# Performance work log

Measured on AMD Instinct MI355X. Metric: run time of the kernel, lower is better.

## Reference

```python
import jax, jax.numpy as jnp
import numpy as np
import math

D_MODEL = 512
N_HEADS = 8
WINDOW = 5
B, S = 4, 2048


def setup_inputs() -> dict:
    key = jax.random.key(0)
    ks = jax.random.split(key, 16)
    d = D_MODEL

    def lin(k, fan_in, fan_out):
        bound = 1.0 / math.sqrt(fan_in)
        kw, kb = jax.random.split(k)
        W = jax.random.uniform(kw, (fan_in, fan_out), jnp.float32, -bound, bound)
        b = jax.random.uniform(kb, (fan_out,), jnp.float32, -bound, bound)
        return W, b

    x = jax.random.normal(ks[0], (B, S, d), jnp.float32)
    W1, b1 = lin(ks[1], d, 2 * d)      # mapping layer 1
    W2, b2 = lin(ks[2], 2 * d, d)      # mapping layer 2
    Wq, bq = lin(ks[3], d, d)
    Wk, bk = lin(ks[4], d, d)
    Wv, bv = lin(ks[5], d, d)
    Wo, bo = lin(ks[6], d, d)
    return dict(x=x, W1=W1, b1=b1, W2=W2, b2=b2, Wq=Wq, bq=bq,
                Wk=Wk, bk=bk, Wv=Wv, bv=bv, Wo=Wo, bo=bo)


def reference(x, W1, b1, W2, b2, Wq, bq, Wk, bk, Wv, bv, Wo, bo):
    Bsz, S_, d = x.shape
    h = N_HEADS
    hd = d // h

    # mapping MLP: Linear -> ReLU -> Linear
    xm = jax.nn.relu(x @ W1 + b1) @ W2 + b2

    def split_heads(t):  # [B,S,d] -> [B,h,S,hd]
        return t.reshape(Bsz, S_, h, hd).transpose(0, 2, 1, 3)

    Q = split_heads(xm @ Wq + bq)
    K = split_heads(xm @ Wk + bk)
    V = split_heads(xm @ Wv + bv)

    scores = jnp.einsum('bhqd,bhkd->bhqk', Q, K) / math.sqrt(hd)

    # inverse sliding-window mask: positions with |i-j| <= window are EXCLUDED
    idx = jnp.arange(S_)
    adjacent = jnp.abs(idx[:, None] - idx[None, :]) <= WINDOW  # [S,S] bool
    scores = jnp.where(adjacent[None, None], -1e9, scores)

    attn = jax.nn.softmax(scores, axis=-1)
    out = jnp.einsum('bhqk,bhkd->bhqd', attn, V)
    out = out.transpose(0, 2, 1, 3).reshape(Bsz, S_, d)
    return out @ Wo + bo
```

## Files before the change

### kernel.cpp

```cpp
#include <hip/hip_runtime.h>
#include <stdint.h>

typedef __attribute__((ext_vector_type(8))) short bf16x8;
typedef __attribute__((ext_vector_type(4))) float f32x4;

__device__ __forceinline__ float bf2f(uint16_t u) {
    union { uint32_t u; float f; } c; c.u = ((uint32_t)u) << 16; return c.f;
}
__device__ __forceinline__ uint16_t f2bf(float f) {
    union { float f; uint32_t u; } c; c.f = f;
    uint32_t r = c.u + 0x7fffu + ((c.u >> 16) & 1u);
    return (uint16_t)(r >> 16);
}
__device__ __forceinline__ uint32_t pk2bf(float a, float b) {
#if __has_builtin(__builtin_amdgcn_cvt_pk_bf16_f32)
    auto v = __builtin_amdgcn_cvt_pk_bf16_f32(a, b);
    uint32_t u; __builtin_memcpy(&u, &v, 4); return u;
#else
    return (uint32_t)f2bf(a) | ((uint32_t)f2bf(b) << 16);
#endif
}
__device__ __forceinline__ float fexp2(float x) {
#if __has_builtin(__builtin_amdgcn_exp2f)
    return __builtin_amdgcn_exp2f(x);
#else
    return exp2f(x);
#endif
}

__device__ __forceinline__ void gld_lds16(const uint16_t* g, uint16_t* l) {
    __builtin_amdgcn_global_load_lds(
        (const __attribute__((address_space(1))) void*)g,
        (__attribute__((address_space(3))) void*)l, 16, 0, 0);
}

__global__ void prep_all(const float* __restrict__ x,
                         const float* __restrict__ W1, const float* __restrict__ W2,
                         const float* __restrict__ Wq, const float* __restrict__ Wk,
                         const float* __restrict__ Wv, const float* __restrict__ Wo,
                         const float* __restrict__ b1, const float* __restrict__ b2,
                         const float* __restrict__ bq, const float* __restrict__ bk,
                         const float* __restrict__ bv, const float* __restrict__ bo,
                         uint16_t* __restrict__ W1T, uint16_t* __restrict__ W2T,
                         uint16_t* __restrict__ WqkvT, uint16_t* __restrict__ WoT,
                         uint16_t* __restrict__ xb, uint16_t* __restrict__ bbase)
{
    const int id = blockIdx.x;
    const int tx = threadIdx.x, ty = threadIdx.y;
    const int tid = ty * 32 + tx;
    if (id < 2048) {
        __shared__ uint16_t t[32][33];
        const float* src; uint16_t* dst; int R, C, tile;
        if      (id < 512)  { src = W1; dst = W1T;              R = 512;  C = 1024; tile = id; }
        else if (id < 1024) { src = W2; dst = W2T;              R = 1024; C = 512;  tile = id - 512; }
        else if (id < 1280) { src = Wq; dst = WqkvT;            R = 512;  C = 512;  tile = id - 1024; }
        else if (id < 1536) { src = Wk; dst = WqkvT + 512*512;  R = 512;  C = 512;  tile = id - 1280; }
        else if (id < 1792) { src = Wv; dst = WqkvT + 1024*512; R = 512;  C = 512;  tile = id - 1536; }
        else                { src = Wo; dst = WoT;              R = 512;  C = 512;  tile = id - 1792; }
        const int ntx = C / 32;
        const int bx = (tile % ntx) * 32, by = (tile / ntx) * 32;
#pragma unroll
        for (int i = ty; i < 32; i += 8) t[i][tx] = f2bf(src[(size_t)(by + i) * C + bx + tx]);
        __syncthreads();
#pragma unroll
        for (int i = ty; i < 32; i += 8) dst[(size_t)(bx + i) * R + by + tx] = t[tx][i];
    } else if (id < 6144) {
        int i = (id - 2048) * 256 + tid;
        float4 v = ((const float4*)x)[i];
        ushort4 o;
        o.x = f2bf(v.x); o.y = f2bf(v.y); o.z = f2bf(v.z); o.w = f2bf(v.w);
        ((ushort4*)xb)[i] = o;
    } else {
        int i = (id - 6144) * 256 + tid;
        if      (i < 1024) bbase[i] = f2bf(b1[i]);
        else if (i < 1536) bbase[i] = f2bf(b2[i - 1024]);
        else if (i < 2048) bbase[i] = f2bf(bq[i - 1536]);
        else if (i < 2560) bbase[i] = f2bf(bk[i - 2048]);
        else if (i < 3072) bbase[i] = f2bf(bv[i - 2560]);
        else if (i < 3584) bbase[i] = f2bf(bo[i - 3072]);
    }
}

template<int RELU, int F32OUT>
__global__ __launch_bounds__(256)
void gemm_k(const uint16_t* __restrict__ A, const uint16_t* __restrict__ Bt,
            const uint16_t* __restrict__ bias, void* __restrict__ Cv,
            int M, int N, int K)
{
    __shared__ __align__(16) uint16_t lsA[128 * 64];
    __shared__ __align__(16) uint16_t lsB[128 * 64];

    const int tid = threadIdx.x, lane = tid & 63;
    const int wid = tid >> 6;
    const int quad = lane >> 4, lm = lane & 15;
    const int wm = wid >> 1, wn = wid & 1;
    const int m0 = blockIdx.y * 128, n0 = blockIdx.x * 128;

    f32x4 acc[4][4];
#pragma unroll
    for (int i = 0; i < 4; ++i)
#pragma unroll
        for (int j = 0; j < 4; ++j) acc[i][j] = (f32x4){0.f, 0.f, 0.f, 0.f};

    for (int k0 = 0; k0 < K; k0 += 64) {
        __syncthreads();
#pragma unroll
        for (int c4 = 0; c4 < 4; ++c4) {
            const int chunk = c4 * 256 + tid;
            const int r = chunk >> 3, lc = (chunk & 7) ^ (r & 7);
            gld_lds16(A  + (size_t)(m0 + r) * K + k0 + lc * 8, lsA + (size_t)chunk * 8);
            gld_lds16(Bt + (size_t)(n0 + r) * K + k0 + lc * 8, lsB + (size_t)chunk * 8);
        }
        __syncthreads();

#pragma unroll
        for (int kh = 0; kh < 2; ++kh) {
            bf16x8 af[4], bfr[4];
#pragma unroll
            for (int t = 0; t < 4; ++t) {
                const int pcA = ((kh * 4 + quad) ^ (lm & 7));
                af[t]  = *(const bf16x8*)(lsA + (wm * 64 + t * 16 + lm) * 64 + pcA * 8);
                bfr[t] = *(const bf16x8*)(lsB + (wn * 64 + t * 16 + lm) * 64 + pcA * 8);
            }
#pragma unroll
            for (int i = 0; i < 4; ++i)
#pragma unroll
                for (int j = 0; j < 4; ++j)
                    acc[i][j] = __builtin_amdgcn_mfma_f32_16x16x32_bf16(af[i], bfr[j], acc[i][j], 0, 0, 0);
        }
    }

#pragma unroll
    for (int i = 0; i < 4; ++i) {
        const int r0 = m0 + wm * 64 + i * 16 + quad * 4;
#pragma unroll
        for (int j = 0; j < 4; ++j) {
            const int col = n0 + wn * 64 + j * 16 + lm;
            const float bvj = bf2f(bias[col]);
#pragma unroll
            for (int r = 0; r < 4; ++r) {
                float v = acc[i][j][r] + bvj;
                if (RELU) v = fmaxf(v, 0.f);
                if (F32OUT) ((float*)Cv)[(size_t)(r0 + r) * N + col] = v;
                else        ((uint16_t*)Cv)[(size_t)(r0 + r) * N + col] = f2bf(v);
            }
        }
    }
}

template<int RELU, int F32OUT>
__global__ __launch_bounds__(256)
void gemm_k64(const uint16_t* __restrict__ A, const uint16_t* __restrict__ Bt,
              const uint16_t* __restrict__ bias, void* __restrict__ Cv,
              int M, int N, int K)
{
    __shared__ __align__(16) uint16_t lsA[64 * 64];
    __shared__ __align__(16) uint16_t lsB[128 * 64];

    const int tid = threadIdx.x, lane = tid & 63;
    const int wid = tid >> 6;
    const int quad = lane >> 4, lm = lane & 15;
    const int wm = wid >> 1, wn = wid & 1;
    const int m0 = blockIdx.y * 64, n0 = blockIdx.x * 128;

    f32x4 acc[2][4];
#pragma unroll
    for (int i = 0; i < 2; ++i)
#pragma unroll
        for (int j = 0; j < 4; ++j) acc[i][j] = (f32x4){0.f, 0.f, 0.f, 0.f};

    for (int k0 = 0; k0 < K; k0 += 64) {
        __syncthreads();
#pragma unroll
        for (int c4 = 0; c4 < 2; ++c4) {
            const int chunk = c4 * 256 + tid;
            const int r = chunk >> 3, lc = (chunk & 7) ^ (r & 7);
            gld_lds16(A + (size_t)(m0 + r) * K + k0 + lc * 8, lsA + (size_t)chunk * 8);
        }
#pragma unroll
        for (int c4 = 0; c4 < 4; ++c4) {
            const int chunk = c4 * 256 + tid;
            const int r = chunk >> 3, lc = (chunk & 7) ^ (r & 7);
            gld_lds16(Bt + (size_t)(n0 + r) * K + k0 + lc * 8, lsB + (size_t)chunk * 8);
        }
        __syncthreads();

#pragma unroll
        for (int kh = 0; kh < 2; ++kh) {
            const int pc = ((kh * 4 + quad) ^ (lm & 7));
            bf16x8 af[2], bfr[4];
#pragma unroll
            for (int t = 0; t < 2; ++t)
                af[t] = *(const bf16x8*)(lsA + (wm * 32 + t * 16 + lm) * 64 + pc * 8);
#pragma unroll
            for (int t = 0; t < 4; ++t)
                bfr[t] = *(const bf16x8*)(lsB + (wn * 64 + t * 16 + lm) * 64 + pc * 8);
#pragma unroll
            for (int i = 0; i < 2; ++i)
#pragma unroll
                for (int j = 0; j < 4; ++j)
                    acc[i][j] = __builtin_amdgcn_mfma_f32_16x16x32_bf16(af[i], bfr[j], acc[i][j], 0, 0, 0);
        }
    }

#pragma unroll
    for (int i = 0; i < 2; ++i) {
        const int r0 = m0 + wm * 32 + i * 16 + quad * 4;
#pragma unroll
        for (int j = 0; j < 4; ++j) {
            const int col = n0 + wn * 64 + j * 16 + lm;
            const float bvj = bf2f(bias[col]);
#pragma unroll
            for (int r = 0; r < 4; ++r) {
                float v = acc[i][j][r] + bvj;
                if (RELU) v = fmaxf(v, 0.f);
                if (F32OUT) ((float*)Cv)[(size_t)(r0 + r) * N + col] = v;
                else        ((uint16_t*)Cv)[(size_t)(r0 + r) * N + col] = f2bf(v);
            }
        }
    }
}

__global__ __launch_bounds__(256)
void gemm_qkv_s(const uint16_t* __restrict__ A, const uint16_t* __restrict__ Bt,
                const uint16_t* __restrict__ bq, const uint16_t* __restrict__ bk,
                const uint16_t* __restrict__ bv_,
                uint16_t* __restrict__ qk, uint16_t* __restrict__ Vt)
{
    __shared__ __align__(16) uint16_t lsA[128 * 64];
    __shared__ __align__(16) uint16_t lsB[128 * 64];

    const int tid = threadIdx.x, lane = tid & 63;
    const int wid = tid >> 6;
    const int quad = lane >> 4, lm = lane & 15;
    const int wm = wid >> 1, wn = wid & 1;
    const int m0 = blockIdx.y * 128, n0 = blockIdx.x * 128;
    const int part = n0 >> 9;
    const uint16_t* B = (part == 0) ? bq : (part == 1) ? bk : bv_;
    const int K = 512;

    f32x4 acc[4][4];
#pragma unroll
    for (int i = 0; i < 4; ++i)
#pragma unroll
        for (int j = 0; j < 4; ++j) acc[i][j] = (f32x4){0.f, 0.f, 0.f, 0.f};

    for (int k0 = 0; k0 < K; k0 += 64) {
        __syncthreads();
#pragma unroll
        for (int c4 = 0; c4 < 4; ++c4) {
            const int chunk = c4 * 256 + tid;
            const int r = chunk >> 3, lc = (chunk & 7) ^ (r & 7);
            gld_lds16(A  + (size_t)(m0 + r) * K + k0 + lc * 8, lsA + (size_t)chunk * 8);
            gld_lds16(Bt + (size_t)(n0 + r) * K + k0 + lc * 8, lsB + (size_t)chunk * 8);
        }
        __syncthreads();

#pragma unroll
        for (int kh = 0; kh < 2; ++kh) {
            const int pc = ((kh * 4 + quad) ^ (lm & 7));
            bf16x8 af[4], bfr[4];
#pragma unroll
            for (int t = 0; t < 4; ++t) {
                af[t]  = *(const bf16x8*)(lsA + (wm * 64 + t * 16 + lm) * 64 + pc * 8);
                bfr[t] = *(const bf16x8*)(lsB + (wn * 64 + t * 16 + lm) * 64 + pc * 8);
            }
#pragma unroll
            for (int i = 0; i < 4; ++i)
#pragma unroll
                for (int j = 0; j < 4; ++j)
                    acc[i][j] = __builtin_amdgcn_mfma_f32_16x16x32_bf16(af[i], bfr[j], acc[i][j], 0, 0, 0);
        }
    }

#pragma unroll
    for (int i = 0; i < 4; ++i) {
        const int mb = m0 + wm * 64 + i * 16 + quad * 4;
#pragma unroll
        for (int j = 0; j < 4; ++j) {
            const int nl = (n0 & 511) + wn * 64 + j * 16 + lm;
            const float bvj = bf2f(B[nl]);
            if (part < 2) {
#pragma unroll
                for (int r = 0; r < 4; ++r)
                    qk[(size_t)(mb + r) * 1024 + part * 512 + nl] = f2bf(acc[i][j][r] + bvj);
            } else {
                const int h = nl >> 6, d = nl & 63;
                const int b = mb >> 11, s0 = mb & 2047;
                const int sp = (s0 & ~31) | ((s0 & 12) << 1) | (((s0 >> 4) & 1) << 2);
                const size_t base = ((size_t)(((b << 3) | h)) * 64 + d) * 2048 + sp;
#pragma unroll
                for (int r = 0; r < 4; ++r)
                    Vt[base + r] = f2bf(acc[i][j][r] + bvj);
            }
        }
    }
}

__global__ __launch_bounds__(256, 3)
void attn_k(const uint16_t* __restrict__ qk, const uint16_t* __restrict__ Vt,
            uint16_t* __restrict__ Out)
{
    __shared__ __align__(16) uint16_t lsK[128 * 64];
    __shared__ __align__(16) uint16_t lsV[64 * 128];

    const int tid = threadIdx.x, lane = tid & 63, wid = tid >> 6;
    const int quad = lane >> 4, lm = lane & 15;
    const int bh = blockIdx.y, b = bh >> 3, h = bh & 7;
    const int q0 = blockIdx.x * 128;
    const float cscale = 0.125f * 1.44269504088896f;

    bf16x8 qf[2][2];
#pragma unroll
    for (int i = 0; i < 2; ++i)
#pragma unroll
        for (int ks = 0; ks < 2; ++ks) {
            bf16x8 q = *(const bf16x8*)(qk +
                (size_t)(b * 2048 + q0 + wid * 32 + i * 16 + lm) * 1024 + h * 64 + ks * 32 + quad * 8);
#pragma unroll
            for (int e = 0; e < 8; ++e)
                q[e] = (short)f2bf(bf2f((uint16_t)q[e]) * cscale);
            qf[i][ks] = q;
        }

    f32x4 oacc[2][4];
#pragma unroll
    for (int i = 0; i < 2; ++i)
#pragma unroll
        for (int n = 0; n < 4; ++n) oacc[i][n] = (f32x4){0.f, 0.f, 0.f, 0.f};
    float lrow[2] = {0.f, 0.f};

    for (int j0 = 0; j0 < 2048; j0 += 128) {
        __syncthreads();
#pragma unroll
        for (int c4 = 0; c4 < 4; ++c4) {
            const int chunk = c4 * 256 + tid;
            const int r = chunk >> 3, lc = (chunk & 7) ^ (r & 7);
            gld_lds16(qk + (size_t)(b * 2048 + j0 + r) * 1024 + 512 + h * 64 + lc * 8,
                      lsK + (size_t)chunk * 8);
        }
#pragma unroll
        for (int c4 = 0; c4 < 4; ++c4) {
            const int chunk = c4 * 256 + tid;
            const int d = chunk >> 4, lc = (chunk & 15) ^ (d & 15);
            gld_lds16(Vt + (size_t)(bh * 64 + d) * 2048 + j0 + lc * 8,
                      lsV + (size_t)chunk * 8);
        }
        __syncthreads();

        f32x4 sacc[2][8];
#pragma unroll
        for (int i = 0; i < 2; ++i)
#pragma unroll
            for (int j = 0; j < 8; ++j) sacc[i][j] = (f32x4){0.f, 0.f, 0.f, 0.f};
#pragma unroll
        for (int ks = 0; ks < 2; ++ks)
#pragma unroll
            for (int j = 0; j < 8; ++j) {
                const int pc = (ks * 4 + quad) ^ (lm & 7);
                bf16x8 kf = *(const bf16x8*)(lsK + (j * 16 + lm) * 64 + pc * 8);
#pragma unroll
                for (int i = 0; i < 2; ++i)
                    sacc[i][j] = __builtin_amdgcn_mfma_f32_16x16x32_bf16(kf, qf[i][ks], sacc[i][j], 0, 0, 0);
            }

        if ((j0 + 127 >= q0 - 5) && (j0 <= q0 + 127 + 5)) {
#pragma unroll
            for (int i = 0; i < 2; ++i) {
                const int qr = q0 + wid * 32 + i * 16 + lm;
#pragma unroll
                for (int j = 0; j < 8; ++j)
#pragma unroll
                    for (int r = 0; r < 4; ++r) {
                        int kc = j0 + j * 16 + quad * 4 + r;
                        int dd = qr - kc; if (dd < 0) dd = -dd;
                        if (dd <= 5) sacc[i][j][r] = -1e30f;
                    }
            }
        }

#pragma unroll
        for (int ks = 0; ks < 4; ++ks) {
            bf16x8 pa[2];
#pragma unroll
            for (int i = 0; i < 2; ++i) {
                const float p0 = fexp2(sacc[i][2 * ks + 0][0]);
                const float p1 = fexp2(sacc[i][2 * ks + 0][1]);
                const float p2 = fexp2(sacc[i][2 * ks + 0][2]);
                const float p3 = fexp2(sacc[i][2 * ks + 0][3]);
                const float p4 = fexp2(sacc[i][2 * ks + 1][0]);
                const float p5 = fexp2(sacc[i][2 * ks + 1][1]);
                const float p6 = fexp2(sacc[i][2 * ks + 1][2]);
                const float p7 = fexp2(sacc[i][2 * ks + 1][3]);
                lrow[i] += ((p0 + p1) + (p2 + p3)) + ((p4 + p5) + (p6 + p7));
                union { bf16x8 v; uint32_t u[4]; } c;
                c.u[0] = pk2bf(p0, p1);
                c.u[1] = pk2bf(p2, p3);
                c.u[2] = pk2bf(p4, p5);
                c.u[3] = pk2bf(p6, p7);
                pa[i] = c.v;
            }
#pragma unroll
            for (int n = 0; n < 4; ++n) {
                const int pc = (ks * 4 + quad) ^ lm;
                bf16x8 vf = *(const bf16x8*)(lsV + (n * 16 + lm) * 128 + pc * 8);
#pragma unroll
                for (int i = 0; i < 2; ++i)
                    oacc[i][n] = __builtin_amdgcn_mfma_f32_16x16x32_bf16(pa[i], vf, oacc[i][n], 0, 0, 0);
            }
        }
    }

#pragma unroll
    for (int i = 0; i < 2; ++i) {
        float l = lrow[i];
        l += __shfl_xor(l, 16);
        l += __shfl_xor(l, 32);
        const float inv = 1.f / (l + 1e-30f);
#pragma unroll
        for (int r = 0; r < 4; ++r) {
            const float invr = __shfl(inv, quad * 4 + r, 16);
            const int s = q0 + wid * 32 + i * 16 + quad * 4 + r;
#pragma unroll
            for (int n = 0; n < 4; ++n)
                Out[(size_t)(b * 2048 + s) * 512 + h * 64 + n * 16 + lm] = f2bf(oacc[i][n][r] * invr);
        }
    }
}

extern "C" void kernel_launch(void* const* d_in, const int* in_sizes, int n_in,
                              void* d_out, int out_size, void* d_ws, size_t ws_size,
                              hipStream_t stream)
{
    const float* x  = (const float*)d_in[0];
    const float* W1 = (const float*)d_in[1];
    const float* b1 = (const float*)d_in[2];
    const float* W2 = (const float*)d_in[3];
    const float* b2 = (const float*)d_in[4];
    const float* Wq = (const float*)d_in[5];
    const float* bq = (const float*)d_in[6];
    const float* Wk = (const float*)d_in[7];
    const float* bk = (const float*)d_in[8];
    const float* Wv = (const float*)d_in[9];
    const float* bv = (const float*)d_in[10];
    const float* Wo = (const float*)d_in[11];
    const float* bo = (const float*)d_in[12];
    (void)in_sizes; (void)n_in; (void)out_size; (void)ws_size;

    char* ws = (char*)d_ws;
    const size_t MiB = 1024 * 1024;
    uint16_t* xb    = (uint16_t*)(ws + 0);
    uint16_t* W1T   = (uint16_t*)(ws + 8 * MiB);
    uint16_t* W2T   = (uint16_t*)(ws + 9 * MiB);
    uint16_t* WqkvT = (uint16_t*)(ws + 10 * MiB);
    uint16_t* WoT   = (uint16_t*)(ws + 11 * MiB + 512 * 1024);
    uint16_t* bbase = (uint16_t*)(ws + 12 * MiB);
    uint16_t* b1b = bbase, *b2b = bbase + 1024, *bqb = bbase + 1536;
    uint16_t* bkb = bbase + 2048, *bvb = bbase + 2560, *bob = bbase + 3072;
    uint16_t* xm1   = (uint16_t*)(ws + 13 * MiB);
    uint16_t* xm    = (uint16_t*)(ws + 29 * MiB);
    uint16_t* qk    = xm1;
    uint16_t* att   = xm;
    uint16_t* Vt    = xb;

    prep_all<<<6158, dim3(32, 8), 0, stream>>>(x, W1, W2, Wq, Wk, Wv, Wo,
                                               b1, b2, bq, bk, bv, bo,
                                               W1T, W2T, WqkvT, WoT, xb, bbase);

    gemm_k<1,0>  <<<dim3(8, 64),  256, 0, stream>>>(xb,  W1T, b1b, xm1, 8192, 1024, 512);
    gemm_k64<0,0><<<dim3(4, 128), 256, 0, stream>>>(xm1, W2T, b2b, xm,  8192, 512, 1024);
    gemm_qkv_s   <<<dim3(12, 64), 256, 0, stream>>>(xm, WqkvT, bqb, bkb, bvb, qk, Vt);
    attn_k       <<<dim3(16, 32), 256, 0, stream>>>(qk, Vt, att);
    gemm_k64<0,1><<<dim3(4, 128), 256, 0, stream>>>(att, WoT, bob, d_out, 8192, 512, 512);
}
```

Before: 228.4 us.

## Double-buffer K/V tiles in LDS with async prefetch and MFMA priority hints

```diff
diff --git a/kernel.cpp b/kernel.cpp
--- a/kernel.cpp
+++ b/kernel.cpp
@@ -297,12 +297,12 @@
     }
 }
 
-__global__ __launch_bounds__(256, 3)
+__global__ __launch_bounds__(256, 2)
 void attn_k(const uint16_t* __restrict__ qk, const uint16_t* __restrict__ Vt,
             uint16_t* __restrict__ Out)
 {
-    __shared__ __align__(16) uint16_t lsK[128 * 64];
-    __shared__ __align__(16) uint16_t lsV[64 * 128];
+    __shared__ __align__(16) uint16_t lsK[2][128 * 64];
+    __shared__ __align__(16) uint16_t lsV[2][64 * 128];
 
     const int tid = threadIdx.x, lane = tid & 63, wid = tid >> 6;
     const int quad = lane >> 4, lm = lane & 15;
@@ -330,39 +330,44 @@
         for (int n = 0; n < 4; ++n) oacc[i][n] = (f32x4){0.f, 0.f, 0.f, 0.f};
     float lrow[2] = {0.f, 0.f};
 
-    for (int j0 = 0; j0 < 2048; j0 += 128) {
-        __syncthreads();
+    auto stage = [&](int j0, int bb) {
 #pragma unroll
         for (int c4 = 0; c4 < 4; ++c4) {
             const int chunk = c4 * 256 + tid;
             const int r = chunk >> 3, lc = (chunk & 7) ^ (r & 7);
             gld_lds16(qk + (size_t)(b * 2048 + j0 + r) * 1024 + 512 + h * 64 + lc * 8,
-                      lsK + (size_t)chunk * 8);
+                      &lsK[bb][(size_t)chunk * 8]);
         }
 #pragma unroll
         for (int c4 = 0; c4 < 4; ++c4) {
             const int chunk = c4 * 256 + tid;
             const int d = chunk >> 4, lc = (chunk & 15) ^ (d & 15);
             gld_lds16(Vt + (size_t)(bh * 64 + d) * 2048 + j0 + lc * 8,
-                      lsV + (size_t)chunk * 8);
-        }
-        __syncthreads();
+                      &lsV[bb][(size_t)chunk * 8]);
+        }
+    };
+
+    auto compute = [&](int j0, int bb) {
+        const uint16_t* Kb = &lsK[bb][0];
+        const uint16_t* Vb = &lsV[bb][0];
 
         f32x4 sacc[2][8];
 #pragma unroll
         for (int i = 0; i < 2; ++i)
 #pragma unroll
             for (int j = 0; j < 8; ++j) sacc[i][j] = (f32x4){0.f, 0.f, 0.f, 0.f};
+        __builtin_amdgcn_s_setprio(1);
 #pragma unroll
         for (int ks = 0; ks < 2; ++ks)
 #pragma unroll
             for (int j = 0; j < 8; ++j) {
                 const int pc = (ks * 4 + quad) ^ (lm & 7);
-                bf16x8 kf = *(const bf16x8*)(lsK + (j * 16 + lm) * 64 + pc * 8);
+                bf16x8 kf = *(const bf16x8*)(Kb + (j * 16 + lm) * 64 + pc * 8);
 #pragma unroll
                 for (int i = 0; i < 2; ++i)
                     sacc[i][j] = __builtin_amdgcn_mfma_f32_16x16x32_bf16(kf, qf[i][ks], sacc[i][j], 0, 0, 0);
             }
+        __builtin_amdgcn_s_setprio(0);
 
         if ((j0 + 127 >= q0 - 5) && (j0 <= q0 + 127 + 5)) {
 #pragma unroll
@@ -400,16 +405,35 @@
                 c.u[3] = pk2bf(p6, p7);
                 pa[i] = c.v;
             }
+            __builtin_amdgcn_s_setprio(1);
 #pragma unroll
             for (int n = 0; n < 4; ++n) {
                 const int pc = (ks * 4 + quad) ^ lm;
-                bf16x8 vf = *(const bf16x8*)(lsV + (n * 16 + lm) * 128 + pc * 8);
+                bf16x8 vf = *(const bf16x8*)(Vb + (n * 16 + lm) * 128 + pc * 8);
 #pragma unroll
                 for (int i = 0; i < 2; ++i)
                     oacc[i][n] = __builtin_amdgcn_mfma_f32_16x16x32_bf16(pa[i], vf, oacc[i][n], 0, 0, 0);
             }
-        }
-    }
+            __builtin_amdgcn_s_setprio(0);
+        }
+    };
+
+    stage(0, 0);
+    int cur = 0;
+#pragma unroll 1
+    for (int jt = 0; jt < 15; ++jt) {
+        stage((jt + 1) * 128, cur ^ 1);
+        asm volatile("s_waitcnt vmcnt(8)" ::: "memory");
+        __builtin_amdgcn_sched_barrier(0);
+        __builtin_amdgcn_s_barrier();
+        compute(jt * 128, cur);
+        __builtin_amdgcn_s_barrier();
+        cur ^= 1;
+    }
+    asm volatile("s_waitcnt vmcnt(0)" ::: "memory");
+    __builtin_amdgcn_sched_barrier(0);
+    __builtin_amdgcn_s_barrier();
+    compute(15 * 128, cur);
 
 #pragma unroll
     for (int i = 0; i < 2; ++i) {
```

New measurement: 217.2 us. 1.05x faster.
